# Kernel optimization log

Hardware: AMD Instinct MI355X
Metric: run time of the kernel (lower is better)

Reference implementation:

```python
import jax, jax.numpy as jnp
import numpy as np


def setup_inputs() -> dict:
    key = jax.random.key(0)
    ks = jax.random.split(key, 8)
    B, L, C = 8, 4096, 1024
    H = C // 2
    return {
        "x": jax.random.normal(ks[0], (B, L, C), dtype=jnp.float32),
        "w1": jax.random.normal(ks[1], (C, 1), dtype=jnp.float32) * 0.02,
        "b1": jnp.zeros((1,), dtype=jnp.float32),
        "w2": jax.random.normal(ks[2], (C, H), dtype=jnp.float32) * 0.02,
        "b2": jnp.zeros((H,), dtype=jnp.float32),
        "w3": jax.random.normal(ks[3], (H, C), dtype=jnp.float32) * 0.02,
        "b3": jnp.zeros((C,), dtype=jnp.float32),
        "w4": jax.random.normal(ks[4], (C, H), dtype=jnp.float32) * 0.02,
        "b4": jnp.zeros((H,), dtype=jnp.float32),
        "w5": jax.random.normal(ks[5], (C, H), dtype=jnp.float32) * 0.02,
        "b5": jnp.zeros((H,), dtype=jnp.float32),
    }


def reference(x, w1, b1, w2, b2, w3, b3, w4, b4, w5, b5):
    # Polarized self-attention (keras): channel branch then spatial branch.
    B, L, C = x.shape
    # --- channel branch ---
    t1 = x @ w1 + b1                                   # conv1: [B, L, 1]
    t2 = x @ w2 + b2                                   # conv2: [B, L, C/2]
    a = jax.nn.softmax(t1.reshape(B, 1, L), axis=-1)   # reshape1 + softmax: [B, 1, L]
    t2 = jnp.einsum('bol,blh->boh', a, t2)             # dot1 (axes 2,1): [B, 1, C/2]
    t2 = jax.nn.sigmoid(t2 @ w3 + b3)                  # conv3 + sigmoid: [B, 1, C]
    # attention1([inputs, t2]): dot scores [B, L, 1]; softmax over key axis of
    # size 1 is exactly 1.0, so output is t2 broadcast across L (exact math).
    o = jnp.broadcast_to(t2, (B, L, C))                # [B, L, C]
    # --- spatial branch ---
    t1 = o @ w4 + b4                                   # conv4: [B, L, C/2]
    t2 = o @ w5 + b5                                   # conv5: [B, L, C/2]
    t1 = jnp.max(t1, axis=1)[:, :, None]               # global max pool + reshape2: [B, C/2, 1]
    s = jax.nn.sigmoid(jnp.einsum('bho,blh->bol', t1, t2))  # dot2 (axes 1,2) + sigmoid: [B, 1, L]
    # attention2([reshape(o, [B,C,L]), s]): scores [B, C, 1]; softmax over the
    # size-1 key axis is 1.0, so output is s broadcast to [B, C, L] (exact).
    out = jnp.broadcast_to(s, (B, C, L)).reshape(B, L, C)  # reshape4
    return out
```

## Files before the change

### kernel.cpp

```cpp
#include <hip/hip_runtime.h>
#include <stdint.h>

#define B 8
#define L 4096
#define C 1024
#define H 512
#define CCH 64
#define WAVES_PER_BATCH 256
#define NPART (B * WAVES_PER_BATCH)

__global__ __launch_bounds__(256) void kA_fused(const float* __restrict__ x,
                                                const float* __restrict__ w1,
                                                const float* __restrict__ b1,
                                                float* __restrict__ partial_xa,
                                                float* __restrict__ partial_s) {
    int waveId = (blockIdx.x << 2) | ((int)threadIdx.x >> 6);
    int lane = threadIdx.x & 63;
    int b = waveId >> 8;
    int chunk = waveId & 255;
    int l0 = chunk * 16;
    float b1v = b1[0];

    const float4* w1v = (const float4*)w1;
    float4 wf[4];
#pragma unroll
    for (int k = 0; k < 4; ++k) wf[k] = w1v[lane + 64 * k];

    float4 acc[4];
#pragma unroll
    for (int k = 0; k < 4; ++k) acc[k] = make_float4(0.f, 0.f, 0.f, 0.f);
    float sexp = 0.f;

    for (int r = 0; r < 16; ++r) {
        const float4* row = (const float4*)(x + ((size_t)(b * L + l0 + r)) * C);
        float4 xv[4];
#pragma unroll
        for (int k = 0; k < 4; ++k) xv[k] = row[lane + 64 * k];
        float d = 0.f;
#pragma unroll
        for (int k = 0; k < 4; ++k)
            d += xv[k].x * wf[k].x + xv[k].y * wf[k].y + xv[k].z * wf[k].z + xv[k].w * wf[k].w;
#pragma unroll
        for (int off = 32; off > 0; off >>= 1) d += __shfl_xor(d, off, 64);
        float e = __expf(d + b1v);
        sexp += e;
#pragma unroll
        for (int k = 0; k < 4; ++k) {
            acc[k].x += e * xv[k].x;
            acc[k].y += e * xv[k].y;
            acc[k].z += e * xv[k].z;
            acc[k].w += e * xv[k].w;
        }
    }
    float4* pxa = (float4*)partial_xa + (size_t)waveId * (C / 4);
#pragma unroll
    for (int k = 0; k < 4; ++k) pxa[lane + 64 * k] = acc[k];
    if (lane == 0) partial_s[waveId] = sexp;
}

__global__ __launch_bounds__(256) void kB_reduce(const float* __restrict__ partial_xa,
                                                 const float* __restrict__ partial_s,
                                                 float* __restrict__ xa,
                                                 float* __restrict__ zero_targets) {
    __shared__ float sred[256];
    __shared__ float4 red[8][32];
    int blk = blockIdx.x, t = threadIdx.x;
    int b = blk >> 3;
    int cg = blk & 7;

    int zi = blk * 256 + t;
    if (zi < 3 * B * H) zero_targets[zi] = 0.f;

    sred[t] = partial_s[b * WAVES_PER_BATCH + t];
    __syncthreads();
    for (int s = 128; s > 0; s >>= 1) { if (t < s) sred[t] += sred[t + s]; __syncthreads(); }
    float inv = 1.f / sred[0];
    __syncthreads();

    int col4 = cg * 32 + (t & 31);
    int rg = t >> 5;
    const float4* pxa = (const float4*)partial_xa;
    float4 a = make_float4(0.f, 0.f, 0.f, 0.f);
    for (int r = 0; r < 32; ++r) {
        float4 v = pxa[(size_t)(b * WAVES_PER_BATCH + rg * 32 + r) * (C / 4) + col4];
        a.x += v.x; a.y += v.y; a.z += v.z; a.w += v.w;
    }
    red[rg][t & 31] = a;
    __syncthreads();
    if (rg == 0) {
        float4 s4 = red[0][t & 31];
#pragma unroll
        for (int g = 1; g < 8; ++g) {
            float4 v = red[g][t & 31];
            s4.x += v.x; s4.y += v.y; s4.z += v.z; s4.w += v.w;
        }
        s4.x *= inv; s4.y *= inv; s4.z *= inv; s4.w *= inv;
        ((float4*)xa)[(size_t)b * (C / 4) + col4] = s4;
    }
}

__global__ __launch_bounds__(256) void k4a_pooled(const float* __restrict__ xa,
                                                  const float* __restrict__ w2,
                                                  const float* __restrict__ b2,
                                                  float* __restrict__ pooled) {
    __shared__ float xs[B][CCH];
    int hg = blockIdx.x & 1;
    int cc = blockIdx.x >> 1;
    int t = threadIdx.x;
    int c0 = cc * CCH;
    for (int i = t; i < B * CCH; i += 256) {
        int bb = i / CCH, ci = i % CCH;
        xs[bb][ci] = xa[bb * C + c0 + ci];
    }
    __syncthreads();
    int h = hg * 256 + t;
    float acc[B] = {0.f, 0.f, 0.f, 0.f, 0.f, 0.f, 0.f, 0.f};
#pragma unroll 4
    for (int ci = 0; ci < CCH; ++ci) {
        float w = w2[(size_t)(c0 + ci) * H + h];
#pragma unroll
        for (int bb = 0; bb < B; ++bb) acc[bb] += xs[bb][ci] * w;
    }
    float bias = (cc == 0) ? b2[h] : 0.f;
#pragma unroll
    for (int bb = 0; bb < B; ++bb) atomicAdd(&pooled[bb * H + h], acc[bb] + bias);
}

__global__ __launch_bounds__(256) void k4bc(const float* __restrict__ pooled,
                                            const float* __restrict__ w3,
                                            const float* __restrict__ b3,
                                            const float* __restrict__ w4,
                                            const float* __restrict__ w5,
                                            float* __restrict__ u4raw,
                                            float* __restrict__ u5raw) {
    __shared__ float pooledS[B][H];
    __shared__ float vpart[4][B][CCH];
    __shared__ float vs[B][CCH];
    int hg = blockIdx.x & 1;
    int cc = blockIdx.x >> 1;
    int c0 = cc * CCH;
    int t = threadIdx.x;

    for (int i = t; i < B * H; i += 256) ((float*)pooledS)[i] = pooled[i];
    __syncthreads();

    {
        int ci = t & 63;
        int hq = t >> 6;
        float a[B] = {0.f, 0.f, 0.f, 0.f, 0.f, 0.f, 0.f, 0.f};
        for (int hh = 0; hh < 128; ++hh) {
            int h = hq * 128 + hh;
            float w = w3[(size_t)h * C + c0 + ci];
#pragma unroll
            for (int bb = 0; bb < B; ++bb) a[bb] += pooledS[bb][h] * w;
        }
#pragma unroll
        for (int bb = 0; bb < B; ++bb) vpart[hq][bb][ci] = a[bb];
    }
    __syncthreads();
#pragma unroll
    for (int p = 0; p < 2; ++p) {
        int idx = t * 2 + p;
        int bb = idx >> 6, ci = idx & 63;
        float v = vpart[0][bb][ci] + vpart[1][bb][ci] + vpart[2][bb][ci] + vpart[3][bb][ci]
                + b3[c0 + ci];
        vs[bb][ci] = 1.f / (1.f + __expf(-v));
    }
    __syncthreads();
    {
        int h = hg * 256 + t;
        float a4[B] = {0.f, 0.f, 0.f, 0.f, 0.f, 0.f, 0.f, 0.f};
        float a5[B] = {0.f, 0.f, 0.f, 0.f, 0.f, 0.f, 0.f, 0.f};
#pragma unroll 2
        for (int ci = 0; ci < CCH; ++ci) {
            float wa = w4[(size_t)(c0 + ci) * H + h];
            float wb = w5[(size_t)(c0 + ci) * H + h];
#pragma unroll
            for (int bb = 0; bb < B; ++bb) {
                a4[bb] += vs[bb][ci] * wa;
                a5[bb] += vs[bb][ci] * wb;
            }
        }
#pragma unroll
        for (int bb = 0; bb < B; ++bb) {
            atomicAdd(&u4raw[bb * H + h], a4[bb]);
            atomicAdd(&u5raw[bb * H + h], a5[bb]);
        }
    }
}

__global__ __launch_bounds__(256) void k5_fill(const float* __restrict__ u4raw, const float* __restrict__ b4,
                                               const float* __restrict__ u5raw, const float* __restrict__ b5,
                                               float* __restrict__ out) {
    __shared__ float red[256];
    int blk = blockIdx.x, t = threadIdx.x;
    int b = blk >> 9;
    int rg = blk & 511;
    float s = (u4raw[b * H + t] + b4[t]) * (u5raw[b * H + t] + b5[t])
            + (u4raw[b * H + 256 + t] + b4[256 + t]) * (u5raw[b * H + 256 + t] + b5[256 + t]);
    red[t] = s; __syncthreads();
    for (int st = 128; st > 0; st >>= 1) { if (t < st) red[t] += red[t + st]; __syncthreads(); }
    float sc = 1.f / (1.f + __expf(-red[0]));
    float4 s4 = make_float4(sc, sc, sc, sc);
    float4* o = (float4*)out + (size_t)b * (L * C / 4) + rg * 2048;
#pragma unroll
    for (int k = 0; k < 8; ++k) o[t + 256 * k] = s4;
}

extern "C" void kernel_launch(void* const* d_in, const int* in_sizes, int n_in,
                              void* d_out, int out_size, void* d_ws, size_t ws_size,
                              hipStream_t stream) {
    const float* x  = (const float*)d_in[0];
    const float* w1 = (const float*)d_in[1];
    const float* b1 = (const float*)d_in[2];
    const float* w2 = (const float*)d_in[3];
    const float* b2 = (const float*)d_in[4];
    const float* w3 = (const float*)d_in[5];
    const float* b3 = (const float*)d_in[6];
    const float* w4 = (const float*)d_in[7];
    const float* b4 = (const float*)d_in[8];
    const float* w5 = (const float*)d_in[9];
    const float* b5 = (const float*)d_in[10];

    float* ws         = (float*)d_ws;
    float* partial_xa = ws;
    float* partial_s  = partial_xa + NPART * C;
    float* xa         = partial_s + NPART;
    float* pooled     = xa + B * C;
    float* u4raw      = pooled + B * H;
    float* u5raw      = u4raw + B * H;

    kA_fused<<<NPART / 4, 256, 0, stream>>>(x, w1, b1, partial_xa, partial_s);
    kB_reduce<<<64, 256, 0, stream>>>(partial_xa, partial_s, xa, pooled);
    k4a_pooled<<<32, 256, 0, stream>>>(xa, w2, b2, pooled);
    k4bc<<<32, 256, 0, stream>>>(pooled, w3, b3, w4, w5, u4raw, u5raw);
    k5_fill<<<B * 512, 256, 0, stream>>>(u4raw, b4, u5raw, b5, (float*)d_out);
}
```

Measured before the change: 311.9 us.

## Reduce partials in-block via LDS and fold reduce kernel into pooled GEMV

```diff
diff --git a/kernel.cpp b/kernel.cpp
--- a/kernel.cpp
+++ b/kernel.cpp
@@ -6,20 +6,24 @@
 #define C 1024
 #define H 512
 #define CCH 64
-#define WAVES_PER_BATCH 256
-#define NPART (B * WAVES_PER_BATCH)
+#define NPART 512
 
 __global__ __launch_bounds__(256) void kA_fused(const float* __restrict__ x,
                                                 const float* __restrict__ w1,
                                                 const float* __restrict__ b1,
                                                 float* __restrict__ partial_xa,
-                                                float* __restrict__ partial_s) {
-    int waveId = (blockIdx.x << 2) | ((int)threadIdx.x >> 6);
-    int lane = threadIdx.x & 63;
-    int b = waveId >> 8;
-    int chunk = waveId & 255;
-    int l0 = chunk * 16;
+                                                float* __restrict__ partial_s,
+                                                float* __restrict__ zero_targets) {
+    __shared__ float4 lds[4][256];
+    __shared__ float ldsS[4];
+    int t = threadIdx.x;
+    int wave = t >> 6, lane = t & 63;
+    int b = blockIdx.x >> 6;
+    int blkInB = blockIdx.x & 63;
+    int l0 = blkInB * 64 + wave * 16;
     float b1v = b1[0];
+
+    if (blockIdx.x < 48) zero_targets[blockIdx.x * 256 + t] = 0.f;
 
     const float4* w1v = (const float4*)w1;
     float4 wf[4];
@@ -52,67 +56,54 @@
             acc[k].w += e * xv[k].w;
         }
     }
-    float4* pxa = (float4*)partial_xa + (size_t)waveId * (C / 4);
-#pragma unroll
-    for (int k = 0; k < 4; ++k) pxa[lane + 64 * k] = acc[k];
-    if (lane == 0) partial_s[waveId] = sexp;
-}
-
-__global__ __launch_bounds__(256) void kB_reduce(const float* __restrict__ partial_xa,
-                                                 const float* __restrict__ partial_s,
-                                                 float* __restrict__ xa,
-                                                 float* __restrict__ zero_targets) {
-    __shared__ float sred[256];
-    __shared__ float4 red[8][32];
-    int blk = blockIdx.x, t = threadIdx.x;
-    int b = blk >> 3;
-    int cg = blk & 7;
-
-    int zi = blk * 256 + t;
-    if (zi < 3 * B * H) zero_targets[zi] = 0.f;
-
-    sred[t] = partial_s[b * WAVES_PER_BATCH + t];
-    __syncthreads();
-    for (int s = 128; s > 0; s >>= 1) { if (t < s) sred[t] += sred[t + s]; __syncthreads(); }
-    float inv = 1.f / sred[0];
-    __syncthreads();
-
-    int col4 = cg * 32 + (t & 31);
-    int rg = t >> 5;
-    const float4* pxa = (const float4*)partial_xa;
-    float4 a = make_float4(0.f, 0.f, 0.f, 0.f);
-    for (int r = 0; r < 32; ++r) {
-        float4 v = pxa[(size_t)(b * WAVES_PER_BATCH + rg * 32 + r) * (C / 4) + col4];
-        a.x += v.x; a.y += v.y; a.z += v.z; a.w += v.w;
-    }
-    red[rg][t & 31] = a;
-    __syncthreads();
-    if (rg == 0) {
-        float4 s4 = red[0][t & 31];
-#pragma unroll
-        for (int g = 1; g < 8; ++g) {
-            float4 v = red[g][t & 31];
-            s4.x += v.x; s4.y += v.y; s4.z += v.z; s4.w += v.w;
-        }
-        s4.x *= inv; s4.y *= inv; s4.z *= inv; s4.w *= inv;
-        ((float4*)xa)[(size_t)b * (C / 4) + col4] = s4;
-    }
-}
-
-__global__ __launch_bounds__(256) void k4a_pooled(const float* __restrict__ xa,
+#pragma unroll
+    for (int k = 0; k < 4; ++k) lds[wave][lane + 64 * k] = acc[k];
+    if (lane == 0) ldsS[wave] = sexp;
+    __syncthreads();
+    float4 s0 = lds[0][t], s1 = lds[1][t], s2 = lds[2][t], s3 = lds[3][t];
+    float4 s4;
+    s4.x = (s0.x + s1.x) + (s2.x + s3.x);
+    s4.y = (s0.y + s1.y) + (s2.y + s3.y);
+    s4.z = (s0.z + s1.z) + (s2.z + s3.z);
+    s4.w = (s0.w + s1.w) + (s2.w + s3.w);
+    ((float4*)partial_xa)[(size_t)blockIdx.x * 256 + t] = s4;
+    if (t == 0) partial_s[blockIdx.x] = (ldsS[0] + ldsS[1]) + (ldsS[2] + ldsS[3]);
+}
+
+__global__ __launch_bounds__(256) void k4a_pooled(const float* __restrict__ partial_xa,
+                                                  const float* __restrict__ partial_s,
                                                   const float* __restrict__ w2,
                                                   const float* __restrict__ b2,
                                                   float* __restrict__ pooled) {
+    __shared__ float ldsS[512];
+    __shared__ float invS[B];
     __shared__ float xs[B][CCH];
     int hg = blockIdx.x & 1;
     int cc = blockIdx.x >> 1;
+    int c0 = cc * CCH;
     int t = threadIdx.x;
-    int c0 = cc * CCH;
-    for (int i = t; i < B * CCH; i += 256) {
-        int bb = i / CCH, ci = i % CCH;
-        xs[bb][ci] = xa[bb * C + c0 + ci];
-    }
-    __syncthreads();
+
+    ldsS[t] = partial_s[t];
+    ldsS[t + 256] = partial_s[t + 256];
+    __syncthreads();
+    if (t < B) {
+        float s = 0.f;
+        for (int i = 0; i < 64; ++i) s += ldsS[t * 64 + i];
+        invS[t] = 1.f / s;
+    }
+    __syncthreads();
+
+#pragma unroll
+    for (int p = 0; p < 2; ++p) {
+        int e = t + p * 256;
+        int bb = e >> 6, ci = e & 63;
+        float s = 0.f;
+        const float* src = partial_xa + (size_t)(bb * 64) * C + c0 + ci;
+        for (int j = 0; j < 64; ++j) s += src[(size_t)j * C];
+        xs[bb][ci] = s * invS[bb];
+    }
+    __syncthreads();
+
     int h = hg * 256 + t;
     float acc[B] = {0.f, 0.f, 0.f, 0.f, 0.f, 0.f, 0.f, 0.f};
 #pragma unroll 4
@@ -194,17 +185,17 @@
                                                float* __restrict__ out) {
     __shared__ float red[256];
     int blk = blockIdx.x, t = threadIdx.x;
-    int b = blk >> 9;
-    int rg = blk & 511;
+    int b = blk >> 8;
+    int rg = blk & 255;
     float s = (u4raw[b * H + t] + b4[t]) * (u5raw[b * H + t] + b5[t])
             + (u4raw[b * H + 256 + t] + b4[256 + t]) * (u5raw[b * H + 256 + t] + b5[256 + t]);
     red[t] = s; __syncthreads();
     for (int st = 128; st > 0; st >>= 1) { if (t < st) red[t] += red[t + st]; __syncthreads(); }
     float sc = 1.f / (1.f + __expf(-red[0]));
     float4 s4 = make_float4(sc, sc, sc, sc);
-    float4* o = (float4*)out + (size_t)b * (L * C / 4) + rg * 2048;
-#pragma unroll
-    for (int k = 0; k < 8; ++k) o[t + 256 * k] = s4;
+    float4* o = (float4*)out + (size_t)b * (L * C / 4) + (size_t)rg * 4096;
+#pragma unroll
+    for (int k = 0; k < 16; ++k) o[t + 256 * k] = s4;
 }
 
 extern "C" void kernel_launch(void* const* d_in, const int* in_sizes, int n_in,
@@ -225,14 +216,12 @@
     float* ws         = (float*)d_ws;
     float* partial_xa = ws;
     float* partial_s  = partial_xa + NPART * C;
-    float* xa         = partial_s + NPART;
-    float* pooled     = xa + B * C;
+    float* pooled     = partial_s + NPART;
     float* u4raw      = pooled + B * H;
     float* u5raw      = u4raw + B * H;
 
-    kA_fused<<<NPART / 4, 256, 0, stream>>>(x, w1, b1, partial_xa, partial_s);
-    kB_reduce<<<64, 256, 0, stream>>>(partial_xa, partial_s, xa, pooled);
-    k4a_pooled<<<32, 256, 0, stream>>>(xa, w2, b2, pooled);
+    kA_fused<<<NPART, 256, 0, stream>>>(x, w1, b1, partial_xa, partial_s, pooled);
+    k4a_pooled<<<32, 256, 0, stream>>>(partial_xa, partial_s, w2, b2, pooled);
     k4bc<<<32, 256, 0, stream>>>(pooled, w3, b3, w4, w5, u4raw, u5raw);
-    k5_fill<<<B * 512, 256, 0, stream>>>(u4raw, b4, u5raw, b5, (float*)d_out);
-}
+    k5_fill<<<2048, 256, 0, stream>>>(u4raw, b4, u5raw, b5, (float*)d_out);
+}
```

Result: no change. 313.6 us (+0.5%).
